# Kernel tuning notes

Hardware: AMD Instinct MI355X
Metric: run time of the kernel (lower is better)

The kernel has to match this reference:

```python
import jax, jax.numpy as jnp
import numpy as np

EPS = 1e-12  # F.normalize clamp
GAMMA = 2    # init kwarg gamma


def setup_inputs() -> dict:
    key = jax.random.key(0)
    k1, k2, k3 = jax.random.split(key, 3)
    b, c, h, w = 8, 256, 64, 64
    x = jax.random.normal(k1, (b, c, h, w), dtype=jnp.float32)
    # 1x1 conv (num_layers=1): weight (c_out, c_in), bias (c_out)
    W = jax.random.normal(k2, (c, c), dtype=jnp.float32) * (1.0 / np.sqrt(c))
    bias = jax.random.normal(k3, (c,), dtype=jnp.float32) * 0.01
    return {"x": x, "W": W, "bias": bias}


def reference(x, W, bias):
    b, c, h, w = x.shape
    hw = h * w
    x_flat = x.reshape(b, c, hw)
    # L2-normalize along channel dim (F.normalize, dim=1)
    norm = jnp.sqrt(jnp.sum(x_flat * x_flat, axis=1, keepdims=True))
    x_norm = x_flat / jnp.maximum(norm, EPS)
    # pixel-pixel cosine similarity: (b, hw, hw), then pow(gamma) + relu
    sim = jnp.einsum('bci,bcj->bij', x_norm, x_norm)
    sim = jax.nn.relu(sim ** GAMMA)
    # transform_net: 1x1 conv == per-pixel linear
    t = jnp.einsum('oc,bci->boi', W, x_flat) + bias[None, :, None]
    # propagate transformed features through similarity
    out = jnp.einsum('bci,bij->bcj', t, sim)
    return out.reshape(b, c, h, w)
```

## Files before the change

### kernel.cpp

```cpp
#include <hip/hip_runtime.h>
#include <stdint.h>

#define HW 4096

typedef unsigned short u16;
typedef unsigned int u32;
typedef __attribute__((ext_vector_type(8))) short bf16x8;
typedef __attribute__((ext_vector_type(4))) float f32x4;
typedef __attribute__((address_space(1))) const unsigned int g_u32;
typedef __attribute__((address_space(3))) unsigned int l_u32;

__device__ __forceinline__ u16 f2bf(float f) {
  union { float f; unsigned u; } v; v.f = f;
  unsigned r = v.u + 0x7FFFu + ((v.u >> 16) & 1u);
  return (u16)(r >> 16);
}

__device__ __forceinline__ void gld16(const void* gsrc, void* ldst) {
  __builtin_amdgcn_global_load_lds((g_u32*)(uintptr_t)gsrc, (l_u32*)(uintptr_t)ldst, 16, 0, 0);
}

__global__ void k_wb(const float* __restrict__ W, u16* __restrict__ wb) {
  int g = blockIdx.x * 256 + threadIdx.x;
  float4 v = ((const float4*)W)[g];
  ushort4 o;
  o.x = f2bf(v.x); o.y = f2bf(v.y); o.z = f2bf(v.z); o.w = f2bf(v.w);
  ((ushort4*)wb)[g] = o;
}

__global__ __launch_bounds__(256) void k_xnt(const float* __restrict__ x,
                                             u16* __restrict__ xnt,
                                             float* __restrict__ nrm) {
  __shared__ float xs[256][65];
  __shared__ float part[4][64];
  __shared__ float invs[64];
  int b = blockIdx.x >> 6;
  int i0 = (blockIdx.x & 63) << 6;
  int il = threadIdx.x & 63;
  int q  = threadIdx.x >> 6;
  const float* xb = x + ((size_t)b << 20);
  float s = 0.f;
  #pragma unroll 8
  for (int k = 0; k < 64; ++k) {
    int c = q * 64 + k;
    float v = xb[((size_t)c << 12) + i0 + il];
    xs[c][il] = v;
    s += v * v;
  }
  part[q][il] = s;
  __syncthreads();
  if (q == 0) {
    float tot = part[0][il] + part[1][il] + part[2][il] + part[3][il];
    float n = fmaxf(sqrtf(tot), 1e-12f);
    nrm[(b << 12) + i0 + il] = n;
    invs[il] = 1.0f / n;
  }
  __syncthreads();
  float iv = invs[il];
  u16* dst = xnt + (((size_t)((b << 12) + i0 + il)) << 8) + q * 64;
  #pragma unroll
  for (int h = 0; h < 8; ++h) {
    u32 wv[4];
    #pragma unroll
    for (int e = 0; e < 4; ++e) {
      float lo = xs[q * 64 + h * 8 + 2 * e][il] * iv;
      float hi = xs[q * 64 + h * 8 + 2 * e + 1][il] * iv;
      wv[e] = (u32)f2bf(lo) | ((u32)f2bf(hi) << 16);
    }
    uint4 p; p.x = wv[0]; p.y = wv[1]; p.z = wv[2]; p.w = wv[3];
    *(uint4*)(dst + h * 8) = p;
  }
}

__global__ __launch_bounds__(256) void k_tgemm(const u16* __restrict__ wb,
                                               const u16* __restrict__ xnt,
                                               const float* __restrict__ bias,
                                               const float* __restrict__ nrm,
                                               u16* __restrict__ t) {
  int b = blockIdx.x >> 6;
  int i0 = (blockIdx.x & 63) << 6;
  int w = threadIdx.x >> 6, l = threadIdx.x & 63;
  int lr = l & 15, lq = l >> 4;
  const u16* xb = xnt + (((size_t)((b << 12) + i0)) << 8);
  const f32x4 fz = {0.f, 0.f, 0.f, 0.f};
  f32x4 acc[4][4];
  #pragma unroll
  for (int a = 0; a < 4; ++a)
    #pragma unroll
    for (int c = 0; c < 4; ++c) acc[a][c] = fz;
  #pragma unroll 2
  for (int ks = 0; ks < 8; ++ks) {
    bf16x8 af[4], bfm[4];
    #pragma unroll
    for (int mf = 0; mf < 4; ++mf)
      af[mf] = *(const bf16x8*)(wb + ((64 * w + mf * 16 + lr) << 8) + ks * 32 + lq * 8);
    #pragma unroll
    for (int nf = 0; nf < 4; ++nf)
      bfm[nf] = *(const bf16x8*)(xb + ((nf * 16 + lr) << 8) + ks * 32 + lq * 8);
    #pragma unroll
    for (int mf = 0; mf < 4; ++mf)
      #pragma unroll
      for (int nf = 0; nf < 4; ++nf)
        acc[mf][nf] = __builtin_amdgcn_mfma_f32_16x16x32_bf16(af[mf], bfm[nf], acc[mf][nf], 0, 0, 0);
  }
  float nv[4];
  #pragma unroll
  for (int nf = 0; nf < 4; ++nf) nv[nf] = nrm[(b << 12) + i0 + nf * 16 + lr];
  #pragma unroll
  for (int mf = 0; mf < 4; ++mf) {
    int o = 64 * w + mf * 16 + lq * 4;
    #pragma unroll
    for (int r = 0; r < 4; ++r) {
      float bs = bias[o + r];
      u16* dst = t + (((size_t)((b << 8) + o + r)) << 12) + i0;
      #pragma unroll
      for (int nf = 0; nf < 4; ++nf) {
        float tv = acc[mf][nf][r] * nv[nf] + bs;
        dst[nf * 16 + lr] = f2bf(tv);
      }
    }
  }
}

__global__ __launch_bounds__(512, 2) void k_main(const u16* __restrict__ xnt,
                                                 const u16* __restrict__ tt,
                                                 float* __restrict__ out) {
  __shared__ __align__(16) char lds[98304];
  char* XiB[2]; XiB[0] = lds; XiB[1] = lds + 32768;
  char* PTB[2]; PTB[0] = lds + 65536; PTB[1] = lds + 81920;

  int bid = blockIdx.x;
  int b = bid & 7;
  int jt = bid >> 3;
  int j0 = jt << 7;
  int tid = threadIdx.x;
  int w = tid >> 6, l = tid & 63;
  int lr = l & 15, lq = l >> 4;
  int iwA = w & 1, jwA = w >> 1;
  int cw = w >> 1, jw2 = w & 1;

  const u16* xb = xnt + ((size_t)b << 20);
  const u16* tb = tt  + ((size_t)b << 20);

  bf16x8 xj[2][8];
  #pragma unroll
  for (int jf = 0; jf < 2; ++jf) {
    const u16* p = xb + ((size_t)(j0 + 32 * jwA + jf * 16 + lr) << 8) + lq * 8;
    #pragma unroll
    for (int ks = 0; ks < 8; ++ks)
      xj[jf][ks] = *(const bf16x8*)(p + ks * 32);
  }

  const f32x4 fz = {0.f, 0.f, 0.f, 0.f};
  f32x4 acc[4][4];
  #pragma unroll
  for (int a = 0; a < 4; ++a)
    #pragma unroll
    for (int c = 0; c < 4; ++c) acc[a][c] = fz;

  u32 soff[4];
  #pragma unroll
  for (int q2 = 0; q2 < 4; ++q2)
    soff[q2] = (u32)((q2 * 16 + lr) * 256 + w * 32 + lq * 8);

  auto stageXi = [&](char* dstbase, int tile) {
    int i0s = (tile & 63) << 6;
    const u16* srcb = xb + ((size_t)i0s << 8);
    #pragma unroll
    for (int q2 = 0; q2 < 4; ++q2)
      gld16(srcb + soff[q2], dstbase + (w * 4 + q2) * 1024);
  };

  stageXi(XiB[0], 0);
  asm volatile("s_waitcnt vmcnt(0)" ::: "memory");
  __builtin_amdgcn_s_barrier();

  for (int it = 0; it < 64; ++it) {
    const int cur = it & 1;
    const int i0 = it << 6;
    char* xiC = XiB[cur];
    char* ptC = PTB[cur];

    #pragma unroll
    for (int jf = 0; jf < 2; ++jf)
      #pragma unroll
      for (int ks = 0; ks < 8; ++ks)
        asm volatile("" : "+v"(xj[jf][ks]));

    bf16x8 tfr[4][2];
    #pragma unroll
    for (int mf = 0; mf < 4; ++mf) {
      const u16* pB = tb + ((size_t)(cw * 64 + mf * 16 + lr) << 12) + i0 + lq * 8;
      tfr[mf][0] = *(const bf16x8*)(pB);
      tfr[mf][1] = *(const bf16x8*)(pB + 32);
    }

    stageXi(XiB[cur ^ 1], it + 1);

    f32x4 sacc[2][2];
    sacc[0][0] = fz; sacc[0][1] = fz; sacc[1][0] = fz; sacc[1][1] = fz;
    const char* abase = xiC + iwA * 2048 + l * 16;
    __builtin_amdgcn_s_setprio(1);
    #pragma unroll
    for (int if_ = 0; if_ < 2; ++if_) {
      bf16x8 bfr[8];
      #pragma unroll
      for (int ks = 0; ks < 8; ++ks)
        bfr[ks] = *(const bf16x8*)(abase + if_ * 1024 + ks * 4096);
      #pragma unroll
      for (int ks = 0; ks < 8; ++ks) {
        sacc[if_][0] = __builtin_amdgcn_mfma_f32_16x16x32_bf16(bfr[ks], xj[0][ks], sacc[if_][0], 0, 0, 0);
        sacc[if_][1] = __builtin_amdgcn_mfma_f32_16x16x32_bf16(bfr[ks], xj[1][ks], sacc[if_][1], 0, 0, 0);
      }
    }
    __builtin_amdgcn_s_setprio(0);

    #pragma unroll
    for (int jf = 0; jf < 2; ++jf) {
      int jj = jwA * 2 + jf;
      int Ab = (jj >> 2) * 8192 + iwA * 4096 + (jj & 3) * 1024;
      #pragma unroll
      for (int if_ = 0; if_ < 2; ++if_) {
        f32x4 s = sacc[if_][jf];
        u32 w0 = (u32)f2bf(s[0] * s[0]) | ((u32)f2bf(s[1] * s[1]) << 16);
        u32 w1 = (u32)f2bf(s[2] * s[2]) | ((u32)f2bf(s[3] * s[3]) << 16);
        int off = Ab + (if_ * 2 + (lq >> 1)) * 256 + lr * 16 + ((lq & 1) << 3);
        uint2 val; val.x = w0; val.y = w1;
        *(uint2*)(ptC + off) = val;
      }
    }

    asm volatile("s_waitcnt lgkmcnt(0)" ::: "memory");
    __builtin_amdgcn_sched_barrier(0);
    __builtin_amdgcn_s_barrier();
    __builtin_amdgcn_sched_barrier(0);

    const char* pbase = ptC + jw2 * 8192 + l * 16;
    __builtin_amdgcn_s_setprio(1);
    #pragma unroll
    for (int ks = 0; ks < 2; ++ks) {
      bf16x8 pfr[4];
      #pragma unroll
      for (int nf = 0; nf < 4; ++nf)
        pfr[nf] = *(const bf16x8*)(pbase + ks * 4096 + nf * 1024);
      #pragma unroll
      for (int mf = 0; mf < 4; ++mf)
        #pragma unroll
        for (int nf = 0; nf < 4; ++nf)
          acc[mf][nf] = __builtin_amdgcn_mfma_f32_16x16x32_bf16(tfr[mf][ks], pfr[nf], acc[mf][nf], 0, 0, 0);
    }
    __builtin_amdgcn_s_setprio(0);

    asm volatile("s_waitcnt vmcnt(0)" ::: "memory");
    __builtin_amdgcn_sched_barrier(0);
    __builtin_amdgcn_s_barrier();
    __builtin_amdgcn_sched_barrier(0);
  }

  #pragma unroll
  for (int mf = 0; mf < 4; ++mf) {
    int c = (b << 8) + cw * 64 + mf * 16 + lq * 4;
    #pragma unroll
    for (int nf = 0; nf < 4; ++nf) {
      int j = j0 + jw2 * 64 + nf * 16 + lr;
      float* dst = out + ((size_t)c << 12) + j;
      #pragma unroll
      for (int r = 0; r < 4; ++r)
        dst[(size_t)r << 12] = acc[mf][nf][r];
    }
  }
}

extern "C" void kernel_launch(void* const* d_in, const int* in_sizes, int n_in,
                              void* d_out, int out_size, void* d_ws, size_t ws_size,
                              hipStream_t stream) {
  const float* x    = (const float*)d_in[0];
  const float* W    = (const float*)d_in[1];
  const float* bias = (const float*)d_in[2];
  float* out = (float*)d_out;

  char* ws = (char*)d_ws;
  u16*   xnt = (u16*)(ws);
  u16*   tt  = (u16*)(ws + ((size_t)16 << 20));
  u16*   wb  = (u16*)(ws + ((size_t)32 << 20));
  float* nrm = (float*)(ws + ((size_t)33 << 20));

  hipLaunchKernelGGL(k_wb,    dim3(64),  dim3(256), 0, stream, W, wb);
  hipLaunchKernelGGL(k_xnt,   dim3(512), dim3(256), 0, stream, x, xnt, nrm);
  hipLaunchKernelGGL(k_tgemm, dim3(512), dim3(256), 0, stream, wb, xnt, bias, nrm, tt);
  hipLaunchKernelGGL(k_main,  dim3(256), dim3(512), 0, stream, xnt, tt, out);
}
```

Before: 397.0 us.

## Pass similarity tile through registers via bpermute, halve j-tile, split-K over waves

The main kernel now uses a 64-column j tile with 512 blocks. Each wave computes a 16x32 similarity slice and rearranges it in registers with ds_bpermute into the B-operand layout, so the LDS round-trip and the mid-iteration barrier are gone. The two wave halves each take half of the i-chunk and reduce their partial output accumulators through LDS at the end. The cost is that every wave loads all 256 channel rows of t, which doubles global t traffic per output. Accumulator registers grow to 16 tiles, and occupancy drops to one block per CU.

```diff
diff --git a/kernel.cpp b/kernel.cpp
--- a/kernel.cpp
+++ b/kernel.cpp
@@ -122,46 +122,42 @@
   }
 }
 
-__global__ __launch_bounds__(512, 2) void k_main(const u16* __restrict__ xnt,
+__global__ __launch_bounds__(512, 1) void k_main(const u16* __restrict__ xnt,
                                                  const u16* __restrict__ tt,
                                                  float* __restrict__ out) {
-  __shared__ __align__(16) char lds[98304];
+  __shared__ __align__(16) char lds[65536];
   char* XiB[2]; XiB[0] = lds; XiB[1] = lds + 32768;
-  char* PTB[2]; PTB[0] = lds + 65536; PTB[1] = lds + 81920;
 
   int bid = blockIdx.x;
   int b = bid & 7;
   int jt = bid >> 3;
-  int j0 = jt << 7;
+  int j0 = jt << 6;
   int tid = threadIdx.x;
   int w = tid >> 6, l = tid & 63;
   int lr = l & 15, lq = l >> 4;
-  int iwA = w & 1, jwA = w >> 1;
-  int cw = w >> 1, jw2 = w & 1;
+  int ih = w >> 2;
+  int jw = w & 3;
 
   const u16* xb = xnt + ((size_t)b << 20);
   const u16* tb = tt  + ((size_t)b << 20);
 
-  bf16x8 xj[2][8];
-  #pragma unroll
-  for (int jf = 0; jf < 2; ++jf) {
-    const u16* p = xb + ((size_t)(j0 + 32 * jwA + jf * 16 + lr) << 8) + lq * 8;
+  bf16x8 xj[8];
+  {
+    const u16* p = xb + ((size_t)(j0 + jw * 16 + lr) << 8) + lq * 8;
     #pragma unroll
     for (int ks = 0; ks < 8; ++ks)
-      xj[jf][ks] = *(const bf16x8*)(p + ks * 32);
+      xj[ks] = *(const bf16x8*)(p + ks * 32);
   }
 
   const f32x4 fz = {0.f, 0.f, 0.f, 0.f};
-  f32x4 acc[4][4];
-  #pragma unroll
-  for (int a = 0; a < 4; ++a)
-    #pragma unroll
-    for (int c = 0; c < 4; ++c) acc[a][c] = fz;
+  f32x4 acc[16];
+  #pragma unroll
+  for (int a = 0; a < 16; ++a) acc[a] = fz;
 
   u32 soff[4];
   #pragma unroll
   for (int q2 = 0; q2 < 4; ++q2)
-    soff[q2] = (u32)((q2 * 16 + lr) * 256 + w * 32 + lq * 8);
+    soff[q2] = (u32)(((q2 & 3) * 16 + lr) * 256 + ((w * 4 + q2) >> 2) * 32 + lq * 8);
 
   auto stageXi = [&](char* dstbase, int tile) {
     int i0s = (tile & 63) << 6;
@@ -174,81 +170,77 @@
   stageXi(XiB[0], 0);
   asm volatile("s_waitcnt vmcnt(0)" ::: "memory");
   __builtin_amdgcn_s_barrier();
+
+  int bp0 = (((l >> 4) & 1) * 32 + (l & 15)) * 4;
+  int bp1 = bp0 + 64;
+  int selhi = (l >> 5);
 
   for (int it = 0; it < 64; ++it) {
     const int cur = it & 1;
     const int i0 = it << 6;
     char* xiC = XiB[cur];
-    char* ptC = PTB[cur];
-
-    #pragma unroll
-    for (int jf = 0; jf < 2; ++jf)
+
+    #pragma unroll
+    for (int ks = 0; ks < 8; ++ks) asm volatile("" : "+v"(xj[ks]));
+
+    bf16x8 tfrA[8];
+    #pragma unroll
+    for (int mf = 0; mf < 8; ++mf)
+      tfrA[mf] = *(const bf16x8*)(tb + ((size_t)(mf * 16 + lr) << 12) + i0 + 32 * ih + lq * 8);
+
+    stageXi(XiB[cur ^ 1], it + 1);
+
+    f32x4 s0 = fz, s1 = fz;
+    const char* ab = xiC + (2 * ih) * 1024 + l * 16;
+    __builtin_amdgcn_s_setprio(1);
+    {
+      bf16x8 bfr[8];
+      #pragma unroll
+      for (int ks = 0; ks < 8; ++ks) bfr[ks] = *(const bf16x8*)(ab + ks * 4096);
       #pragma unroll
       for (int ks = 0; ks < 8; ++ks)
-        asm volatile("" : "+v"(xj[jf][ks]));
-
-    bf16x8 tfr[4][2];
-    #pragma unroll
-    for (int mf = 0; mf < 4; ++mf) {
-      const u16* pB = tb + ((size_t)(cw * 64 + mf * 16 + lr) << 12) + i0 + lq * 8;
-      tfr[mf][0] = *(const bf16x8*)(pB);
-      tfr[mf][1] = *(const bf16x8*)(pB + 32);
-    }
-
-    stageXi(XiB[cur ^ 1], it + 1);
-
-    f32x4 sacc[2][2];
-    sacc[0][0] = fz; sacc[0][1] = fz; sacc[1][0] = fz; sacc[1][1] = fz;
-    const char* abase = xiC + iwA * 2048 + l * 16;
+        s0 = __builtin_amdgcn_mfma_f32_16x16x32_bf16(bfr[ks], xj[ks], s0, 0, 0, 0);
+    }
+    {
+      bf16x8 bfr[8];
+      #pragma unroll
+      for (int ks = 0; ks < 8; ++ks) bfr[ks] = *(const bf16x8*)(ab + 1024 + ks * 4096);
+      #pragma unroll
+      for (int ks = 0; ks < 8; ++ks)
+        s1 = __builtin_amdgcn_mfma_f32_16x16x32_bf16(bfr[ks], xj[ks], s1, 0, 0, 0);
+    }
+    __builtin_amdgcn_s_setprio(0);
+
+    bf16x8 tfrB[8];
+    #pragma unroll
+    for (int mf = 0; mf < 8; ++mf)
+      tfrB[mf] = *(const bf16x8*)(tb + ((size_t)((mf + 8) * 16 + lr) << 12) + i0 + 32 * ih + lq * 8);
+
+    u32 pk[2][2];
+    pk[0][0] = (u32)f2bf(s0[0] * s0[0]) | ((u32)f2bf(s0[1] * s0[1]) << 16);
+    pk[1][0] = (u32)f2bf(s0[2] * s0[2]) | ((u32)f2bf(s0[3] * s0[3]) << 16);
+    pk[0][1] = (u32)f2bf(s1[0] * s1[0]) | ((u32)f2bf(s1[1] * s1[1]) << 16);
+    pk[1][1] = (u32)f2bf(s1[2] * s1[2]) | ((u32)f2bf(s1[3] * s1[3]) << 16);
+
+    int bm[4];
+    #pragma unroll
+    for (int m = 0; m < 4; ++m) {
+      int addr = (m < 2) ? bp0 : bp1;
+      int X = __builtin_amdgcn_ds_bpermute(addr, (int)pk[m & 1][0]);
+      int Y = __builtin_amdgcn_ds_bpermute(addr, (int)pk[m & 1][1]);
+      bm[m] = selhi ? Y : X;
+    }
+    union { int4 i; bf16x8 v; } pu;
+    pu.i.x = bm[0]; pu.i.y = bm[1]; pu.i.z = bm[2]; pu.i.w = bm[3];
+    bf16x8 pfr = pu.v;
+
     __builtin_amdgcn_s_setprio(1);
     #pragma unroll
-    for (int if_ = 0; if_ < 2; ++if_) {
-      bf16x8 bfr[8];
-      #pragma unroll
-      for (int ks = 0; ks < 8; ++ks)
-        bfr[ks] = *(const bf16x8*)(abase + if_ * 1024 + ks * 4096);
-      #pragma unroll
-      for (int ks = 0; ks < 8; ++ks) {
-        sacc[if_][0] = __builtin_amdgcn_mfma_f32_16x16x32_bf16(bfr[ks], xj[0][ks], sacc[if_][0], 0, 0, 0);
-        sacc[if_][1] = __builtin_amdgcn_mfma_f32_16x16x32_bf16(bfr[ks], xj[1][ks], sacc[if_][1], 0, 0, 0);
-      }
-    }
-    __builtin_amdgcn_s_setprio(0);
-
-    #pragma unroll
-    for (int jf = 0; jf < 2; ++jf) {
-      int jj = jwA * 2 + jf;
-      int Ab = (jj >> 2) * 8192 + iwA * 4096 + (jj & 3) * 1024;
-      #pragma unroll
-      for (int if_ = 0; if_ < 2; ++if_) {
-        f32x4 s = sacc[if_][jf];
-        u32 w0 = (u32)f2bf(s[0] * s[0]) | ((u32)f2bf(s[1] * s[1]) << 16);
-        u32 w1 = (u32)f2bf(s[2] * s[2]) | ((u32)f2bf(s[3] * s[3]) << 16);
-        int off = Ab + (if_ * 2 + (lq >> 1)) * 256 + lr * 16 + ((lq & 1) << 3);
-        uint2 val; val.x = w0; val.y = w1;
-        *(uint2*)(ptC + off) = val;
-      }
-    }
-
-    asm volatile("s_waitcnt lgkmcnt(0)" ::: "memory");
-    __builtin_amdgcn_sched_barrier(0);
-    __builtin_amdgcn_s_barrier();
-    __builtin_amdgcn_sched_barrier(0);
-
-    const char* pbase = ptC + jw2 * 8192 + l * 16;
-    __builtin_amdgcn_s_setprio(1);
-    #pragma unroll
-    for (int ks = 0; ks < 2; ++ks) {
-      bf16x8 pfr[4];
-      #pragma unroll
-      for (int nf = 0; nf < 4; ++nf)
-        pfr[nf] = *(const bf16x8*)(pbase + ks * 4096 + nf * 1024);
-      #pragma unroll
-      for (int mf = 0; mf < 4; ++mf)
-        #pragma unroll
-        for (int nf = 0; nf < 4; ++nf)
-          acc[mf][nf] = __builtin_amdgcn_mfma_f32_16x16x32_bf16(tfr[mf][ks], pfr[nf], acc[mf][nf], 0, 0, 0);
-    }
+    for (int mf = 0; mf < 8; ++mf)
+      acc[mf] = __builtin_amdgcn_mfma_f32_16x16x32_bf16(tfrA[mf], pfr, acc[mf], 0, 0, 0);
+    #pragma unroll
+    for (int mf = 0; mf < 8; ++mf)
+      acc[mf + 8] = __builtin_amdgcn_mfma_f32_16x16x32_bf16(tfrB[mf], pfr, acc[mf + 8], 0, 0, 0);
     __builtin_amdgcn_s_setprio(0);
 
     asm volatile("s_waitcnt vmcnt(0)" ::: "memory");
@@ -257,16 +249,23 @@
     __builtin_amdgcn_sched_barrier(0);
   }
 
-  #pragma unroll
-  for (int mf = 0; mf < 4; ++mf) {
-    int c = (b << 8) + cw * 64 + mf * 16 + lq * 4;
-    #pragma unroll
-    for (int nf = 0; nf < 4; ++nf) {
-      int j = j0 + jw2 * 64 + nf * 16 + lr;
+  if (ih == 1) {
+    #pragma unroll
+    for (int mf = 0; mf < 16; ++mf)
+      *(f32x4*)(lds + jw * 16384 + mf * 1024 + l * 16) = acc[mf];
+  }
+  asm volatile("s_waitcnt lgkmcnt(0)" ::: "memory");
+  __builtin_amdgcn_s_barrier();
+  if (ih == 0) {
+    #pragma unroll
+    for (int mf = 0; mf < 16; ++mf) {
+      f32x4 part = *(const f32x4*)(lds + jw * 16384 + mf * 1024 + l * 16);
+      int c = (b << 8) + mf * 16 + lq * 4;
+      int j = j0 + jw * 16 + lr;
       float* dst = out + ((size_t)c << 12) + j;
       #pragma unroll
       for (int r = 0; r < 4; ++r)
-        dst[(size_t)r << 12] = acc[mf][nf][r];
+        dst[(size_t)r << 12] = acc[mf][r] + part[r];
     }
   }
 }
@@ -288,5 +287,5 @@
   hipLaunchKernelGGL(k_wb,    dim3(64),  dim3(256), 0, stream, W, wb);
   hipLaunchKernelGGL(k_xnt,   dim3(512), dim3(256), 0, stream, x, xnt, nrm);
   hipLaunchKernelGGL(k_tgemm, dim3(512), dim3(256), 0, stream, wb, xnt, bias, nrm, tt);
-  hipLaunchKernelGGL(k_main,  dim3(256), dim3(512), 0, stream, xnt, tt, out);
-}
+  hipLaunchKernelGGL(k_main,  dim3(512), dim3(512), 0, stream, xnt, tt, out);
+}
```

After: 830.4 us. 109% more time.
